# Performance work log

Measured on AMD Instinct MI355X. Metric: run time of the kernel, lower is better.

## Reference

```python
import jax, jax.numpy as jnp
import numpy as np

EPS = 1e-7  # K.epsilon()

def setup_inputs() -> dict:
    key = jax.random.key(0)
    k1, k2, k3 = jax.random.split(key, 3)
    B, T, D = 32, 2048, 512
    x = jax.random.normal(k1, (B, T, D), dtype=jnp.float32)
    W = jax.random.normal(k2, (D, D), dtype=jnp.float32) * (1.0 / np.sqrt(D))
    b = jnp.zeros((D,), dtype=jnp.float32)
    u = jax.random.normal(k3, (D,), dtype=jnp.float32) * (1.0 / np.sqrt(D))
    return {"x": x, "W": W, "b": b, "u": u}

def reference(x, W, b, u):
    # uit = tanh(x @ W + b)  -> [B, T, D]
    uit = jnp.tanh(jnp.einsum('btd,de->bte', x, W) + b)
    # scores: sum over feature dim of uit * u -> [B, T]
    ait = jnp.einsum('btd,d->bt', uit, u)
    # exp + normalize over T (no mask); matches original exp/sum form
    a = jnp.exp(ait)
    a = a / (jnp.sum(a, axis=1, keepdims=True) + EPS)
    # weighted sum pooling over T -> [B, D]
    return jnp.einsum('btd,bt->bd', x, a)
```

## Files before the change

kernel.cpp:

```cpp
#include <hip/hip_runtime.h>
#include <math.h>

#define D_DIM 512

typedef short short8v __attribute__((ext_vector_type(8)));
typedef unsigned short ushort8v __attribute__((ext_vector_type(8)));
typedef float f32x16 __attribute__((ext_vector_type(16)));

__device__ inline unsigned short f2bf(float f) {
    union { float f; unsigned int u; } a; a.f = f;
    unsigned int u = a.u;
    unsigned int r = (u + 0x7fffu + ((u >> 16) & 1u)) >> 16;
    return (unsigned short)r;
}

__device__ inline float fast_tanh(float y) {
    float e2 = __expf(2.f * y);
    return 1.f - __fdividef(2.f, e2 + 1.f);
}

__global__ __launch_bounds__(256) void wt_kernel(const float* __restrict__ W,
                                                 unsigned short* __restrict__ Wb) {
    int g = blockIdx.x * 256 + threadIdx.x;
    int k = g >> 7;
    int e4 = (g & 127) * 4;
    float4 v = *(const float4*)(W + (size_t)k * D_DIM + e4);
    Wb[(size_t)(e4 + 0) * D_DIM + k] = f2bf(v.x);
    Wb[(size_t)(e4 + 1) * D_DIM + k] = f2bf(v.y);
    Wb[(size_t)(e4 + 2) * D_DIM + k] = f2bf(v.z);
    Wb[(size_t)(e4 + 3) * D_DIM + k] = f2bf(v.w);
}

constexpr int LDE = 40;

__global__ __launch_bounds__(256, 2) void gemm_ait_mfma(
    const float* __restrict__ x, const unsigned short* __restrict__ Wb,
    const float* __restrict__ bias, const float* __restrict__ u,
    float* __restrict__ ait)
{
    __shared__ __align__(16) unsigned short xs[64 * LDE];
    __shared__ __align__(16) unsigned short wsh[512 * LDE];
    __shared__ float rowpart[4][64];

    const int tid  = threadIdx.x;
    const int wave = tid >> 6;
    const int lane = tid & 63;
    const int half = lane >> 5;
    const int nl   = lane & 31;
    const int m0   = blockIdx.x * 64;

    f32x16 acc[2][4];
    #pragma unroll
    for (int mi = 0; mi < 2; ++mi)
        #pragma unroll
        for (int ni = 0; ni < 4; ++ni)
            #pragma unroll
            for (int r = 0; r < 16; ++r) acc[mi][ni][r] = 0.f;

    const int xr = tid >> 2;
    const int xc = tid & 3;
    const float* xbase = x + (size_t)(m0 + xr) * D_DIM + xc * 8;

    int wg_off[8], wl_off[8];
    #pragma unroll
    for (int p = 0; p < 8; ++p) {
        int chunk = tid + p * 256;
        int e  = chunk >> 2;
        int ci = chunk & 3;
        wg_off[p] = e * D_DIM + ci * 8;
        wl_off[p] = e * LDE + ci * 8;
    }

    float4 px0 = *(const float4*)(xbase);
    float4 px1 = *(const float4*)(xbase + 4);
    ushort8v pw[8];
    #pragma unroll
    for (int p = 0; p < 8; ++p)
        pw[p] = *(const ushort8v*)&Wb[wg_off[p]];

    for (int kk = 0; kk < D_DIM; kk += 32) {
        {
            ushort8v pk;
            pk[0] = f2bf(px0.x); pk[1] = f2bf(px0.y); pk[2] = f2bf(px0.z); pk[3] = f2bf(px0.w);
            pk[4] = f2bf(px1.x); pk[5] = f2bf(px1.y); pk[6] = f2bf(px1.z); pk[7] = f2bf(px1.w);
            *(ushort8v*)&xs[xr * LDE + xc * 8] = pk;
        }
        #pragma unroll
        for (int p = 0; p < 8; ++p)
            *(ushort8v*)&wsh[wl_off[p]] = pw[p];
        __syncthreads();

        if (kk + 32 < D_DIM) {
            px0 = *(const float4*)(xbase + kk + 32);
            px1 = *(const float4*)(xbase + kk + 36);
            #pragma unroll
            for (int p = 0; p < 8; ++p)
                pw[p] = *(const ushort8v*)&Wb[wg_off[p] + kk + 32];
        }

        #pragma unroll
        for (int ks = 0; ks < 2; ++ks) {
            short8v af[2], bfr[4];
            #pragma unroll
            for (int mi = 0; mi < 2; ++mi)
                af[mi] = *(const short8v*)&xs[(mi * 32 + nl) * LDE + ks * 16 + half * 8];
            #pragma unroll
            for (int ni = 0; ni < 4; ++ni)
                bfr[ni] = *(const short8v*)&wsh[(wave * 128 + ni * 32 + nl) * LDE + ks * 16 + half * 8];
            #pragma unroll
            for (int mi = 0; mi < 2; ++mi)
                #pragma unroll
                for (int ni = 0; ni < 4; ++ni)
                    acc[mi][ni] = __builtin_amdgcn_mfma_f32_32x32x16_bf16(
                        af[mi], bfr[ni], acc[mi][ni], 0, 0, 0);
        }
        __syncthreads();
    }

    float rowsum[2][16];
    #pragma unroll
    for (int mi = 0; mi < 2; ++mi)
        #pragma unroll
        for (int r = 0; r < 16; ++r) rowsum[mi][r] = 0.f;

    #pragma unroll
    for (int mi = 0; mi < 2; ++mi) {
        #pragma unroll
        for (int ni = 0; ni < 4; ++ni) {
            int col = wave * 128 + ni * 32 + nl;
            float be = bias[col], ue = u[col];
            #pragma unroll
            for (int r = 0; r < 16; ++r)
                rowsum[mi][r] += fast_tanh(acc[mi][ni][r] + be) * ue;
        }
    }
    #pragma unroll
    for (int mi = 0; mi < 2; ++mi)
        #pragma unroll
        for (int r = 0; r < 16; ++r) {
            float v = rowsum[mi][r];
            v += __shfl_xor(v, 1, 64);
            v += __shfl_xor(v, 2, 64);
            v += __shfl_xor(v, 4, 64);
            v += __shfl_xor(v, 8, 64);
            v += __shfl_xor(v, 16, 64);
            rowsum[mi][r] = v;
        }
    if (nl == 0) {
        #pragma unroll
        for (int mi = 0; mi < 2; ++mi)
            #pragma unroll
            for (int r = 0; r < 16; ++r) {
                int row = mi * 32 + (r & 3) + 8 * (r >> 2) + 4 * half;
                rowpart[wave][row] = rowsum[mi][r];
            }
    }
    __syncthreads();
    if (tid < 64)
        ait[m0 + tid] = rowpart[0][tid] + rowpart[1][tid] + rowpart[2][tid] + rowpart[3][tid];
}

__global__ __launch_bounds__(256) void gemm_ait_f32(
    const float* __restrict__ x, const float* __restrict__ W,
    const float* __restrict__ bias, const float* __restrict__ u,
    float* __restrict__ ait)
{
    __shared__ float xsf[64][68];
    __shared__ float wshf[64][132];
    const int tid = threadIdx.x;
    const int tx = tid & 15, ty = tid >> 4;
    const int m0 = blockIdx.x * 64;
    float rowsum[4] = {0.f, 0.f, 0.f, 0.f};
    for (int e0 = 0; e0 < D_DIM; e0 += 128) {
        float acc[4][8];
        #pragma unroll
        for (int i = 0; i < 4; ++i)
            #pragma unroll
            for (int j = 0; j < 8; ++j) acc[i][j] = 0.f;
        for (int kc = 0; kc < D_DIM; kc += 64) {
            #pragma unroll
            for (int i = 0; i < 4; ++i) {
                int idx = tid + i * 256;
                int r = idx >> 4, c = (idx & 15) * 4;
                *(float4*)&xsf[r][c] = *(const float4*)(x + (size_t)(m0 + r) * D_DIM + kc + c);
            }
            #pragma unroll
            for (int i = 0; i < 8; ++i) {
                int idx = tid + i * 256;
                int r = idx >> 5, c = (idx & 31) * 4;
                *(float4*)&wshf[r][c] = *(const float4*)(W + (size_t)(kc + r) * D_DIM + e0 + c);
            }
            __syncthreads();
            #pragma unroll 4
            for (int k = 0; k < 64; ++k) {
                float xv[4];
                #pragma unroll
                for (int i = 0; i < 4; ++i) xv[i] = xsf[ty * 4 + i][k];
                float4 w0 = *(const float4*)&wshf[k][tx * 8];
                float4 w1 = *(const float4*)&wshf[k][tx * 8 + 4];
                #pragma unroll
                for (int i = 0; i < 4; ++i) {
                    acc[i][0] += xv[i] * w0.x; acc[i][1] += xv[i] * w0.y;
                    acc[i][2] += xv[i] * w0.z; acc[i][3] += xv[i] * w0.w;
                    acc[i][4] += xv[i] * w1.x; acc[i][5] += xv[i] * w1.y;
                    acc[i][6] += xv[i] * w1.z; acc[i][7] += xv[i] * w1.w;
                }
            }
            __syncthreads();
        }
        #pragma unroll
        for (int j = 0; j < 8; ++j) {
            int e = e0 + tx * 8 + j;
            float be = bias[e], ue = u[e];
            #pragma unroll
            for (int i = 0; i < 4; ++i) rowsum[i] += tanhf(acc[i][j] + be) * ue;
        }
    }
    float* red = &xsf[0][0];
    #pragma unroll
    for (int i = 0; i < 4; ++i) red[(ty * 4 + i) * 16 + tx] = rowsum[i];
    __syncthreads();
    if (tid < 64) {
        float s = 0.f;
        #pragma unroll
        for (int j = 0; j < 16; ++j) s += red[tid * 16 + j];
        ait[m0 + tid] = s;
    }
}

__global__ __launch_bounds__(256) void softmax_kernel(float* __restrict__ ait, int T)
{
    const int b = blockIdx.x;
    float* p = ait + (size_t)b * T;
    const int tid = threadIdx.x;
    float ev[8];
    float local = 0.f;
    #pragma unroll
    for (int i = 0; i < 8; ++i) {
        ev[i] = expf(p[tid + i * 256]);
        local += ev[i];
    }
    #pragma unroll
    for (int off = 32; off > 0; off >>= 1)
        local += __shfl_down(local, off, 64);
    __shared__ float wsum[4];
    const int wv = tid >> 6, lane = tid & 63;
    if (lane == 0) wsum[wv] = local;
    __syncthreads();
    float total = wsum[0] + wsum[1] + wsum[2] + wsum[3];
    float inv = 1.0f / (total + 1e-7f);
    #pragma unroll
    for (int i = 0; i < 8; ++i) p[tid + i * 256] = ev[i] * inv;
}

__global__ __launch_bounds__(256) void pool_partial_kernel(
    const float* __restrict__ x, const float* __restrict__ a,
    float* __restrict__ partial, int T)
{
    const int chunks = T >> 7;
    const int b = blockIdx.x / chunks;
    const int c = blockIdx.x % chunks;
    const int tid = threadIdx.x;
    const int th = tid >> 7;
    const int d = (tid & 127) * 4;
    const int t0 = c * 128;

    const float* xp = x + ((size_t)b * T + t0) * D_DIM + d;
    const float* ap = a + (size_t)b * T + t0;

    float4 acc = {0.f, 0.f, 0.f, 0.f};
    #pragma unroll 8
    for (int t = th; t < 128; t += 2) {
        float s = ap[t];
        float4 xv = *(const float4*)(xp + (size_t)t * D_DIM);
        acc.x += xv.x * s; acc.y += xv.y * s;
        acc.z += xv.z * s; acc.w += xv.w * s;
    }
    __shared__ float4 tmp[128];
    if (th == 1) tmp[tid & 127] = acc;
    __syncthreads();
    if (th == 0) {
        float4 o = tmp[tid];
        acc.x += o.x; acc.y += o.y; acc.z += o.z; acc.w += o.w;
        *(float4*)(partial + (size_t)blockIdx.x * D_DIM + d) = acc;
    }
}

__global__ __launch_bounds__(256) void pool_reduce_kernel(
    const float* __restrict__ partial, float* __restrict__ out, int chunks)
{
    const int b = blockIdx.x;
    const int tid = threadIdx.x;
    const int d = tid * 2;
    float2 acc = {0.f, 0.f};
    for (int c = 0; c < chunks; ++c) {
        float2 v = *(const float2*)(partial + ((size_t)b * chunks + c) * D_DIM + d);
        acc.x += v.x; acc.y += v.y;
    }
    *(float2*)(out + (size_t)b * D_DIM + d) = acc;
}

__global__ __launch_bounds__(256) void pool_atomic_kernel(
    const float* __restrict__ x, const float* __restrict__ a,
    float* __restrict__ out, int T)
{
    const int chunks = T >> 8;
    const int b = blockIdx.x / chunks;
    const int c = blockIdx.x % chunks;
    const int tid = threadIdx.x;
    const int d = tid * 2;
    const int t0 = c * 256;
    const float* xp = x + ((size_t)b * T + t0) * D_DIM + d;
    const float* ap = a + (size_t)b * T + t0;
    float2 acc = {0.f, 0.f};
    for (int t = 0; t < 256; ++t) {
        float s = ap[t];
        float2 xv = *(const float2*)(xp + (size_t)t * D_DIM);
        acc.x += xv.x * s; acc.y += xv.y * s;
    }
    float* o = out + (size_t)b * D_DIM + d;
    atomicAdd(o + 0, acc.x);
    atomicAdd(o + 1, acc.y);
}

extern "C" void kernel_launch(void* const* d_in, const int* in_sizes, int n_in,
                              void* d_out, int out_size, void* d_ws, size_t ws_size,
                              hipStream_t stream)
{
    const float* x    = (const float*)d_in[0];
    const float* W    = (const float*)d_in[1];
    const float* bias = (const float*)d_in[2];
    const float* u    = (const float*)d_in[3];
    float* out = (float*)d_out;

    const int Dd = in_sizes[2];
    const int M  = in_sizes[0] / Dd;
    const int B  = out_size / Dd;
    const int T  = M / B;
    const int chunks = T >> 7;

    const size_t wb_bytes   = (size_t)Dd * Dd * sizeof(unsigned short);
    const size_t ait_bytes  = (size_t)M * sizeof(float);
    const size_t part_bytes = (size_t)B * chunks * Dd * sizeof(float);

    if (ws_size >= wb_bytes + ait_bytes) {
        unsigned short* Wb = (unsigned short*)d_ws;
        float* ait = (float*)((char*)d_ws + wb_bytes);
        wt_kernel<<<dim3((Dd * Dd / 4) / 256), dim3(256), 0, stream>>>(W, Wb);
        gemm_ait_mfma<<<dim3(M / 64), dim3(256), 0, stream>>>(x, Wb, bias, u, ait);
        softmax_kernel<<<dim3(B), dim3(256), 0, stream>>>(ait, T);
        if (ws_size >= wb_bytes + ait_bytes + part_bytes) {
            float* partial = (float*)((char*)d_ws + wb_bytes + ait_bytes);
            pool_partial_kernel<<<dim3(B * chunks), dim3(256), 0, stream>>>(x, ait, partial, T);
            pool_reduce_kernel<<<dim3(B), dim3(256), 0, stream>>>(partial, out, chunks);
        } else {
            hipMemsetAsync(d_out, 0, (size_t)out_size * sizeof(float), stream);
            pool_atomic_kernel<<<dim3(B * (T >> 8)), dim3(256), 0, stream>>>(x, ait, out, T);
        }
    } else {
        float* ait = (float*)d_ws;
        gemm_ait_f32<<<dim3(M / 64), dim3(256), 0, stream>>>(x, W, bias, u, ait);
        softmax_kernel<<<dim3(B), dim3(256), 0, stream>>>(ait, T);
        hipMemsetAsync(d_out, 0, (size_t)out_size * sizeof(float), stream);
        pool_atomic_kernel<<<dim3(B * (T >> 8)), dim3(256), 0, stream>>>(x, ait, out, T);
    }
}
```

Before: 265.3 us.

## Pre-swizzle W into MFMA layout and double-buffer async global-to-LDS loads

The weight conversion kernel now writes bf16 W in a per-k-slab layout that matches the MFMA B-fragment order, so the GEMM can copy each slab straight into LDS with global_load_lds into a double buffer instead of staging it through registers. This drops the trailing barrier per k-step and frees VGPRs, aiming to overlap weight traffic with MFMA work. Pooling chunks shrink from 128 to 64 timesteps for more blocks, and the atomic fallback now shares the float4 accumulator. LDS use grows to about 70KB per block, which may limit occupancy to 2 blocks per CU or fewer, and there is no explicit wait on the async copies before the barrier.

```diff
diff --git a/kernel.cpp b/kernel.cpp
--- a/kernel.cpp
+++ b/kernel.cpp
@@ -19,27 +19,47 @@
     return 1.f - __fdividef(2.f, e2 + 1.f);
 }
 
+#define ASYNC_CP16(gp, lp) \
+    __builtin_amdgcn_global_load_lds( \
+        (const __attribute__((address_space(1))) void*)(gp), \
+        (__attribute__((address_space(3))) void*)(lp), 16, 0, 0)
+
 __global__ __launch_bounds__(256) void wt_kernel(const float* __restrict__ W,
-                                                 unsigned short* __restrict__ Wb) {
-    int g = blockIdx.x * 256 + threadIdx.x;
-    int k = g >> 7;
-    int e4 = (g & 127) * 4;
-    float4 v = *(const float4*)(W + (size_t)k * D_DIM + e4);
-    Wb[(size_t)(e4 + 0) * D_DIM + k] = f2bf(v.x);
-    Wb[(size_t)(e4 + 1) * D_DIM + k] = f2bf(v.y);
-    Wb[(size_t)(e4 + 2) * D_DIM + k] = f2bf(v.z);
-    Wb[(size_t)(e4 + 3) * D_DIM + k] = f2bf(v.w);
-}
-
-constexpr int LDE = 40;
+                                                 unsigned short* __restrict__ Wb2) {
+    __shared__ __align__(16) unsigned short lbuf[16384];
+    const int s = blockIdx.x;
+    const int tid = threadIdx.x;
+    #pragma unroll
+    for (int i = 0; i < 16; ++i) {
+        int flat = tid + i * 256;
+        int kr = flat >> 7;
+        int e4 = (flat & 127) * 4;
+        float4 v = *(const float4*)(W + (size_t)(s * 32 + kr) * D_DIM + e4);
+        int ks = kr >> 4, half = (kr >> 3) & 1, j = kr & 7;
+        float vv[4] = {v.x, v.y, v.z, v.w};
+        #pragma unroll
+        for (int q = 0; q < 4; ++q) {
+            int e = e4 + q, nt = e >> 5, nl = e & 31;
+            lbuf[(((nt * 2 + ks) * 2 + half) * 32 + nl) * 8 + j] = f2bf(vv[q]);
+        }
+    }
+    __syncthreads();
+    #pragma unroll
+    for (int i = 0; i < 8; ++i) {
+        int c = tid + i * 256;
+        *(ushort8v*)(Wb2 + (size_t)s * 16384 + c * 8) = *(const ushort8v*)&lbuf[c * 8];
+    }
+}
+
+constexpr int XLDE = 40;
 
 __global__ __launch_bounds__(256, 2) void gemm_ait_mfma(
-    const float* __restrict__ x, const unsigned short* __restrict__ Wb,
+    const float* __restrict__ x, const unsigned short* __restrict__ Wb2,
     const float* __restrict__ bias, const float* __restrict__ u,
     float* __restrict__ ait)
 {
-    __shared__ __align__(16) unsigned short xs[64 * LDE];
-    __shared__ __align__(16) unsigned short wsh[512 * LDE];
+    __shared__ __align__(16) unsigned short wsh[2][16384];
+    __shared__ __align__(16) unsigned short xs[2][64 * XLDE];
     __shared__ float rowpart[4][64];
 
     const int tid  = threadIdx.x;
@@ -61,41 +81,29 @@
     const int xc = tid & 3;
     const float* xbase = x + (size_t)(m0 + xr) * D_DIM + xc * 8;
 
-    int wg_off[8], wl_off[8];
-    #pragma unroll
-    for (int p = 0; p < 8; ++p) {
-        int chunk = tid + p * 256;
-        int e  = chunk >> 2;
-        int ci = chunk & 3;
-        wg_off[p] = e * D_DIM + ci * 8;
-        wl_off[p] = e * LDE + ci * 8;
-    }
-
+    #pragma unroll
+    for (int i = 0; i < 8; ++i)
+        ASYNC_CP16(Wb2 + tid * 8 + i * 2048, &wsh[0][tid * 8 + i * 2048]);
     float4 px0 = *(const float4*)(xbase);
     float4 px1 = *(const float4*)(xbase + 4);
-    ushort8v pw[8];
-    #pragma unroll
-    for (int p = 0; p < 8; ++p)
-        pw[p] = *(const ushort8v*)&Wb[wg_off[p]];
-
-    for (int kk = 0; kk < D_DIM; kk += 32) {
+
+    for (int s = 0; s < 16; ++s) {
+        const int pb = s & 1;
         {
             ushort8v pk;
             pk[0] = f2bf(px0.x); pk[1] = f2bf(px0.y); pk[2] = f2bf(px0.z); pk[3] = f2bf(px0.w);
             pk[4] = f2bf(px1.x); pk[5] = f2bf(px1.y); pk[6] = f2bf(px1.z); pk[7] = f2bf(px1.w);
-            *(ushort8v*)&xs[xr * LDE + xc * 8] = pk;
-        }
-        #pragma unroll
-        for (int p = 0; p < 8; ++p)
-            *(ushort8v*)&wsh[wl_off[p]] = pw[p];
+            *(ushort8v*)&xs[pb][xr * XLDE + xc * 8] = pk;
+        }
         __syncthreads();
 
-        if (kk + 32 < D_DIM) {
-            px0 = *(const float4*)(xbase + kk + 32);
-            px1 = *(const float4*)(xbase + kk + 36);
-            #pragma unroll
-            for (int p = 0; p < 8; ++p)
-                pw[p] = *(const ushort8v*)&Wb[wg_off[p] + kk + 32];
+        if (s + 1 < 16) {
+            const unsigned short* wsrc = Wb2 + (size_t)(s + 1) * 16384;
+            #pragma unroll
+            for (int i = 0; i < 8; ++i)
+                ASYNC_CP16(wsrc + tid * 8 + i * 2048, &wsh[1 - pb][tid * 8 + i * 2048]);
+            px0 = *(const float4*)(xbase + (s + 1) * 32);
+            px1 = *(const float4*)(xbase + (s + 1) * 32 + 4);
         }
 
         #pragma unroll
@@ -103,10 +111,10 @@
             short8v af[2], bfr[4];
             #pragma unroll
             for (int mi = 0; mi < 2; ++mi)
-                af[mi] = *(const short8v*)&xs[(mi * 32 + nl) * LDE + ks * 16 + half * 8];
+                af[mi] = *(const short8v*)&xs[pb][(mi * 32 + nl) * XLDE + ks * 16 + half * 8];
             #pragma unroll
             for (int ni = 0; ni < 4; ++ni)
-                bfr[ni] = *(const short8v*)&wsh[(wave * 128 + ni * 32 + nl) * LDE + ks * 16 + half * 8];
+                bfr[ni] = *(const short8v*)&wsh[pb][(((wave * 4 + ni) * 2 + ks) * 2 + half) * 256 + nl * 8];
             #pragma unroll
             for (int mi = 0; mi < 2; ++mi)
                 #pragma unroll
@@ -114,7 +122,6 @@
                     acc[mi][ni] = __builtin_amdgcn_mfma_f32_32x32x16_bf16(
                         af[mi], bfr[ni], acc[mi][ni], 0, 0, 0);
         }
-        __syncthreads();
     }
 
     float rowsum[2][16];
@@ -253,36 +260,40 @@
     for (int i = 0; i < 8; ++i) p[tid + i * 256] = ev[i] * inv;
 }
 
-__global__ __launch_bounds__(256) void pool_partial_kernel(
-    const float* __restrict__ x, const float* __restrict__ a,
-    float* __restrict__ partial, int T)
-{
-    const int chunks = T >> 7;
-    const int b = blockIdx.x / chunks;
-    const int c = blockIdx.x % chunks;
-    const int tid = threadIdx.x;
+__device__ inline float4 pool_accum(const float* __restrict__ x,
+                                    const float* __restrict__ a,
+                                    int b, int c, int tid, int T) {
     const int th = tid >> 7;
     const int d = (tid & 127) * 4;
-    const int t0 = c * 128;
-
-    const float* xp = x + ((size_t)b * T + t0) * D_DIM + d;
-    const float* ap = a + (size_t)b * T + t0;
-
+    const float* xp = x + ((size_t)b * T + c * 64) * D_DIM + d;
+    const float* ap = a + (size_t)b * T + c * 64;
     float4 acc = {0.f, 0.f, 0.f, 0.f};
     #pragma unroll 8
-    for (int t = th; t < 128; t += 2) {
+    for (int t = th; t < 64; t += 2) {
         float s = ap[t];
         float4 xv = *(const float4*)(xp + (size_t)t * D_DIM);
         acc.x += xv.x * s; acc.y += xv.y * s;
         acc.z += xv.z * s; acc.w += xv.w * s;
     }
+    return acc;
+}
+
+__global__ __launch_bounds__(256) void pool_partial_kernel(
+    const float* __restrict__ x, const float* __restrict__ a,
+    float* __restrict__ partial, int T)
+{
+    const int chunks = T >> 6;
+    const int b = blockIdx.x / chunks;
+    const int c = blockIdx.x % chunks;
+    const int tid = threadIdx.x;
+    float4 acc = pool_accum(x, a, b, c, tid, T);
     __shared__ float4 tmp[128];
-    if (th == 1) tmp[tid & 127] = acc;
-    __syncthreads();
-    if (th == 0) {
+    if ((tid >> 7) == 1) tmp[tid & 127] = acc;
+    __syncthreads();
+    if ((tid >> 7) == 0) {
         float4 o = tmp[tid];
         acc.x += o.x; acc.y += o.y; acc.z += o.z; acc.w += o.w;
-        *(float4*)(partial + (size_t)blockIdx.x * D_DIM + d) = acc;
+        *(float4*)(partial + (size_t)blockIdx.x * D_DIM + tid * 4) = acc;
     }
 }
 
@@ -304,23 +315,22 @@
     const float* __restrict__ x, const float* __restrict__ a,
     float* __restrict__ out, int T)
 {
-    const int chunks = T >> 8;
+    const int chunks = T >> 6;
     const int b = blockIdx.x / chunks;
     const int c = blockIdx.x % chunks;
     const int tid = threadIdx.x;
-    const int d = tid * 2;
-    const int t0 = c * 256;
-    const float* xp = x + ((size_t)b * T + t0) * D_DIM + d;
-    const float* ap = a + (size_t)b * T + t0;
-    float2 acc = {0.f, 0.f};
-    for (int t = 0; t < 256; ++t) {
-        float s = ap[t];
-        float2 xv = *(const float2*)(xp + (size_t)t * D_DIM);
-        acc.x += xv.x * s; acc.y += xv.y * s;
-    }
-    float* o = out + (size_t)b * D_DIM + d;
-    atomicAdd(o + 0, acc.x);
-    atomicAdd(o + 1, acc.y);
+    float4 acc = pool_accum(x, a, b, c, tid, T);
+    __shared__ float4 tmp[128];
+    if ((tid >> 7) == 1) tmp[tid & 127] = acc;
+    __syncthreads();
+    if ((tid >> 7) == 0) {
+        float4 o = tmp[tid];
+        float* op = out + (size_t)b * D_DIM + tid * 4;
+        atomicAdd(op + 0, acc.x + o.x);
+        atomicAdd(op + 1, acc.y + o.y);
+        atomicAdd(op + 2, acc.z + o.z);
+        atomicAdd(op + 3, acc.w + o.w);
+    }
 }
 
 extern "C" void kernel_launch(void* const* d_in, const int* in_sizes, int n_in,
@@ -337,17 +347,17 @@
     const int M  = in_sizes[0] / Dd;
     const int B  = out_size / Dd;
     const int T  = M / B;
-    const int chunks = T >> 7;
+    const int chunks = T >> 6;
 
     const size_t wb_bytes   = (size_t)Dd * Dd * sizeof(unsigned short);
     const size_t ait_bytes  = (size_t)M * sizeof(float);
     const size_t part_bytes = (size_t)B * chunks * Dd * sizeof(float);
 
     if (ws_size >= wb_bytes + ait_bytes) {
-        unsigned short* Wb = (unsigned short*)d_ws;
+        unsigned short* Wb2 = (unsigned short*)d_ws;
         float* ait = (float*)((char*)d_ws + wb_bytes);
-        wt_kernel<<<dim3((Dd * Dd / 4) / 256), dim3(256), 0, stream>>>(W, Wb);
-        gemm_ait_mfma<<<dim3(M / 64), dim3(256), 0, stream>>>(x, Wb, bias, u, ait);
+        wt_kernel<<<dim3(16), dim3(256), 0, stream>>>(W, Wb2);
+        gemm_ait_mfma<<<dim3(M / 64), dim3(256), 0, stream>>>(x, Wb2, bias, u, ait);
         softmax_kernel<<<dim3(B), dim3(256), 0, stream>>>(ait, T);
         if (ws_size >= wb_bytes + ait_bytes + part_bytes) {
             float* partial = (float*)((char*)d_ws + wb_bytes + ait_bytes);
@@ -355,13 +365,13 @@
             pool_reduce_kernel<<<dim3(B), dim3(256), 0, stream>>>(partial, out, chunks);
         } else {
             hipMemsetAsync(d_out, 0, (size_t)out_size * sizeof(float), stream);
-            pool_atomic_kernel<<<dim3(B * (T >> 8)), dim3(256), 0, stream>>>(x, ait, out, T);
+            pool_atomic_kernel<<<dim3(B * chunks), dim3(256), 0, stream>>>(x, ait, out, T);
         }
     } else {
         float* ait = (float*)d_ws;
         gemm_ait_f32<<<dim3(M / 64), dim3(256), 0, stream>>>(x, W, bias, u, ait);
         softmax_kernel<<<dim3(B), dim3(256), 0, stream>>>(ait, T);
         hipMemsetAsync(d_out, 0, (size_t)out_size * sizeof(float), stream);
-        pool_atomic_kernel<<<dim3(B * (T >> 8)), dim3(256), 0, stream>>>(x, ait, out, T);
-    }
-}
+        pool_atomic_kernel<<<dim3(B * chunks), dim3(256), 0, stream>>>(x, ait, out, T);
+    }
+}
```

Measured after the change: 274.4 us. +3.4%, slower.
